# Optimization experiments

Hardware: AMD Instinct MI355X
Metric: run time of the kernel (lower is better)

Reference implementation:

```python
import jax, jax.numpy as jnp
import numpy as np

N = 65536   # base nodes
M = 65536   # union local nodes
E = 1048576 # base edges
EL = 1048576 # local edges
K = 131072  # membership entries
F = 128     # in_channels
H = 128     # hidden_dim
L = 2       # num_layers
OUT = 2
ALPHA = 0.9


def setup_inputs() -> dict:
    key = jax.random.key(0)
    ks = jax.random.split(key, 16)
    s = 1.0 / np.sqrt(H)
    return {
        "x": jax.random.normal(ks[0], (N, F), jnp.float32),
        "edge_index": jax.random.randint(ks[1], (2, E), 0, N, jnp.int64 if jax.config.jax_enable_x64 else jnp.int32),
        "edge_weight": jax.random.uniform(ks[2], (E,), jnp.float32),
        "local_x0": jax.random.normal(ks[3], (M, F), jnp.float32),
        "copy2orig": jax.random.randint(ks[4], (M,), 0, N),
        "local_adj_index": jax.random.randint(ks[5], (2, EL), 0, M),
        "local_adj_value": jax.random.uniform(ks[6], (EL,), jnp.float32),
        "memb_idx": jax.random.randint(ks[7], (K,), 0, M),
        "memb_gid": jax.random.randint(ks[8], (K,), 0, 64),
        "B": 64,
        "Wb_in": jax.random.normal(ks[9], (F, H), jnp.float32) * s,
        "bb_in": jnp.zeros((H,), jnp.float32),
        "Wl_in": jax.random.normal(ks[10], (F, H), jnp.float32) * s,
        "bl_in": jnp.zeros((H,), jnp.float32),
        "W_base": jax.random.normal(ks[11], (L, H, H), jnp.float32) * s,
        "b_base": jnp.zeros((L, H), jnp.float32),
        "W_local": jax.random.normal(ks[12], (L, H, H), jnp.float32) * s,
        "b_local": jnp.zeros((L, H), jnp.float32),
        "Wp": jax.random.normal(ks[13], (H, OUT), jnp.float32) * s,
        "bp": jnp.zeros((OUT,), jnp.float32),
    }


def reference(x, edge_index, edge_weight, local_x0, copy2orig, local_adj_index,
              local_adj_value, memb_idx, memb_gid, B, Wb_in, bb_in, Wl_in, bl_in,
              W_base, b_base, W_local, b_local, Wp, bp):
    n = x.shape[0]
    m = local_x0.shape[0]
    # input projections (dropout is identity in eval mode)
    base_x = jax.nn.relu(x @ Wb_in + bb_in)
    local_x = jax.nn.relu(local_x0 @ Wl_in + bl_in)
    src, dst = edge_index[0], edge_index[1]
    lsrc, ldst = local_adj_index[0], local_adj_index[1]
    for l in range(W_base.shape[0]):
        # base graph propagation: normalized-adjacency spmm then linear+relu
        base_agg = jax.ops.segment_sum(base_x[src] * edge_weight[:, None], dst, num_segments=n)
        base_x = jax.nn.relu(base_agg @ W_base[l] + b_base[l])
        # local union-graph propagation + alpha-mix with base features via copy2orig
        local_agg = jax.ops.segment_sum(local_x[lsrc] * local_adj_value[:, None], ldst, num_segments=m)
        mix = ALPHA * local_agg + (1.0 - ALPHA) * base_x[copy2orig]
        local_x = jax.nn.relu(mix @ W_local[l] + b_local[l])
    # scatter-mean pooling by membership (fused sum + count)
    sub = jax.ops.segment_sum(local_x[memb_idx], memb_gid, num_segments=B)
    cnt = jax.ops.segment_sum(jnp.ones((memb_gid.shape[0], 1), local_x.dtype), memb_gid, num_segments=B)
    sub = sub / jnp.maximum(cnt, 1.0)
    return sub @ Wp + bp
```

## Files before the change

kernel.cpp:

```cpp
#include <hip/hip_runtime.h>

typedef __attribute__((ext_vector_type(8))) short bfrag;
typedef __attribute__((ext_vector_type(4))) float ffrag;

__device__ __forceinline__ ushort f2bf(float f) {
    union { float f; unsigned u; } v{f};
    unsigned r = v.u + 0x7fff + ((v.u >> 16) & 1);
    return (ushort)(r >> 16);
}
__device__ __forceinline__ float bf2f(ushort u) {
    union { unsigned u; float f; } v{(unsigned)u << 16};
    return v.f;
}
__device__ __forceinline__ float bflo(unsigned u) {
    union { unsigned u; float f; } v{u << 16};
    return v.f;
}
__device__ __forceinline__ float bfhi(unsigned u) {
    union { unsigned u; float f; } v{u & 0xffff0000u};
    return v.f;
}


__global__ __launch_bounds__(256) void zero_kernel(int* __restrict__ p, int n) {
    int i = blockIdx.x * 256 + threadIdx.x;
    if (i < n) p[i] = 0;
}


__global__ __launch_bounds__(256) void bhist(const int* __restrict__ dst, int* __restrict__ bcount) {
    __shared__ int h[256];
    const int t = threadIdx.x;
    h[t] = 0;
    __syncthreads();
    const int base = blockIdx.x * 4096;
#pragma unroll
    for (int u = 0; u < 16; ++u)
        atomicAdd(&h[((unsigned)dst[base + u * 256 + t]) >> 8], 1);
    __syncthreads();
    atomicAdd(&bcount[t], h[t]);
}

__global__ __launch_bounds__(256) void bscan(const int* __restrict__ bcount, int* __restrict__ bstart,
                                             int* __restrict__ bcursor) {
    __shared__ int s[256];
    const int t = threadIdx.x;
    int c = bcount[t];
    s[t] = c;
    __syncthreads();
    for (int o = 1; o < 256; o <<= 1) {
        int add = (t >= o) ? s[t - o] : 0;
        __syncthreads();
        s[t] += add;
        __syncthreads();
    }
    int excl = s[t] - c;
    bstart[t] = excl;
    bcursor[t] = excl;
    if (t == 255) bstart[256] = s[t];
}

#define CH 4096

__global__ __launch_bounds__(256) void bucket1(const int* __restrict__ src, const int* __restrict__ dst,
                                               const float* __restrict__ w, int* __restrict__ bcursor,
                                               int2* __restrict__ staged) {
    __shared__ int cnt_s[256], base_l[256], base_g[256], cur[256];
    __shared__ int2 stage[CH];
    __shared__ unsigned char bb[CH];
    const int t = threadIdx.x;
    const int base = blockIdx.x * CH;
    cnt_s[t] = 0;
    __syncthreads();
#pragma unroll
    for (int u = 0; u < CH / 256; ++u) {
        int b = ((unsigned)dst[base + u * 256 + t]) >> 8;
        atomicAdd(&cnt_s[b], 1);
    }
    __syncthreads();
    int v = cnt_s[t];
    base_l[t] = v;
    __syncthreads();
    for (int o = 1; o < 256; o <<= 1) {
        int add = (t >= o) ? base_l[t - o] : 0;
        __syncthreads();
        base_l[t] += add;
        __syncthreads();
    }
    int excl = base_l[t] - v;
    base_l[t] = excl;
    cur[t] = excl;
    base_g[t] = atomicAdd(&bcursor[t], v);
    __syncthreads();
#pragma unroll
    for (int u = 0; u < CH / 256; ++u) {
        int e = base + u * 256 + t;
        int d = dst[e];
        int b = ((unsigned)d) >> 8;
        int p = atomicAdd(&cur[b], 1);
        stage[p] = make_int2((src[e] & 0xffff) | ((d & 255) << 16), __float_as_int(w[e]));
        bb[p] = (unsigned char)b;
    }
    __syncthreads();
    for (int i = t; i < CH; i += 256) {
        int b = bb[i];
        staged[base_g[b] + (i - base_l[b])] = stage[i];
    }
}

__global__ __launch_bounds__(256) void bucket2n(const int* __restrict__ bstart, const int2* __restrict__ staged,
                                                int* __restrict__ start, int2* __restrict__ edges) {
    __shared__ int cnt[256], excl[256], cur[256];
    const int t = threadIdx.x;
    const int b = blockIdx.x;
    cnt[t] = 0;
    __syncthreads();
    const int s0 = bstart[b];
    const int s1 = bstart[b + 1];
    for (int i = s0 + t; i < s1; i += 256) {
        int dl = (staged[i].x >> 16) & 0xff;
        atomicAdd(&cnt[dl], 1);
    }
    __syncthreads();
    int v = cnt[t];
    excl[t] = v;
    __syncthreads();
    for (int o = 1; o < 256; o <<= 1) {
        int add = (t >= o) ? excl[t - o] : 0;
        __syncthreads();
        excl[t] += add;
        __syncthreads();
    }
    int e = excl[t] - v;
    cur[t] = e;
    start[b * 256 + t] = s0 + e;
    if (b == 255 && t == 255) start[256 * 256] = s1;
    __syncthreads();
    for (int i = s0 + t; i < s1; i += 256) {
        int2 se = staged[i];
        int dl = (se.x >> 16) & 0xff;
        int p = s0 + atomicAdd(&cur[dl], 1);
        edges[p] = make_int2(se.x & 0xffff, se.y);
    }
}


__global__ __launch_bounds__(256) void wprep(const float* __restrict__ Wb_in, const float* __restrict__ Wl_in,
                                             const float* __restrict__ W_base, const float* __restrict__ W_local,
                                             ushort* __restrict__ out) {
    int idx = blockIdx.x * 256 + threadIdx.x;
    int mat = idx >> 14;
    int i = idx & 16383;
    int nn = i >> 7, kk = i & 127;
    const float* src;
    switch (mat) {
        case 0: src = Wb_in; break;
        case 1: src = Wl_in; break;
        case 2: src = W_base; break;
        case 3: src = W_base + 16384; break;
        case 4: src = W_local; break;
        default: src = W_local + 16384; break;
    }
    out[(size_t)mat * 16384 + i] = f2bf(src[kk * 128 + nn]);
}


#define ASTRIDE 136

template <bool A_F32, bool MIX>
__global__ __launch_bounds__(256) void gemm_mfma(const void* __restrict__ Ap, const ushort* __restrict__ A2,
                                                 const int* __restrict__ ridx,
                                                 const ushort* __restrict__ Wt, const float* __restrict__ bias,
                                                 ushort* __restrict__ Y) {
    __shared__ ushort As[64 * ASTRIDE];
    __shared__ ushort Bs[128 * ASTRIDE];
    const int tid = threadIdx.x;
    const int r0 = blockIdx.x * 64;

    if (A_F32) {
        const float* A = (const float*)Ap;
#pragma unroll
        for (int p = 0; p < 8; ++p) {
            int c = p * 256 + tid;
            int row = c >> 5, o4 = (c & 31) * 4;
            float4 v = *(const float4*)(A + (size_t)(r0 + row) * 128 + o4);
            ushort4 u;
            u.x = f2bf(v.x); u.y = f2bf(v.y); u.z = f2bf(v.z); u.w = f2bf(v.w);
            *(ushort4*)&As[row * ASTRIDE + o4] = u;
        }
    } else {
        const ushort* A = (const ushort*)Ap;
#pragma unroll
        for (int p = 0; p < 4; ++p) {
            int c = p * 256 + tid;
            int row = c >> 4, o8 = (c & 15) * 8;
            uint4 v = *(const uint4*)(A + (size_t)(r0 + row) * 128 + o8);
            if (MIX) {
                int rr = ridx[r0 + row];
                uint4 v2 = *(const uint4*)(A2 + (size_t)rr * 128 + o8);
                uint4 o;
                float x0, x1;
                x0 = 0.9f * bflo(v.x) + 0.1f * bflo(v2.x);
                x1 = 0.9f * bfhi(v.x) + 0.1f * bfhi(v2.x);
                o.x = (unsigned)f2bf(x0) | ((unsigned)f2bf(x1) << 16);
                x0 = 0.9f * bflo(v.y) + 0.1f * bflo(v2.y);
                x1 = 0.9f * bfhi(v.y) + 0.1f * bfhi(v2.y);
                o.y = (unsigned)f2bf(x0) | ((unsigned)f2bf(x1) << 16);
                x0 = 0.9f * bflo(v.z) + 0.1f * bflo(v2.z);
                x1 = 0.9f * bfhi(v.z) + 0.1f * bfhi(v2.z);
                o.z = (unsigned)f2bf(x0) | ((unsigned)f2bf(x1) << 16);
                x0 = 0.9f * bflo(v.w) + 0.1f * bflo(v2.w);
                x1 = 0.9f * bfhi(v.w) + 0.1f * bfhi(v2.w);
                o.w = (unsigned)f2bf(x0) | ((unsigned)f2bf(x1) << 16);
                v = o;
            }
            *(uint4*)&As[row * ASTRIDE + o8] = v;
        }
    }
#pragma unroll
    for (int p = 0; p < 8; ++p) {
        int c = p * 256 + tid;
        int n = c >> 4, o8 = (c & 15) * 8;
        *(uint4*)&Bs[n * ASTRIDE + o8] = *(const uint4*)(Wt + n * 128 + o8);
    }
    __syncthreads();

    const int lane = tid & 63;
    const int w = tid >> 6;
    const int wm = (w & 1) * 32;
    const int wn = (w >> 1) * 64;
    const int q = lane >> 4;
    const int l16 = lane & 15;

    ffrag acc[2][4];
#pragma unroll
    for (int mt = 0; mt < 2; ++mt)
#pragma unroll
        for (int nt = 0; nt < 4; ++nt) acc[mt][nt] = (ffrag){0.f, 0.f, 0.f, 0.f};

#pragma unroll
    for (int kc = 0; kc < 4; ++kc) {
        bfrag a[2], b[4];
#pragma unroll
        for (int mt = 0; mt < 2; ++mt)
            a[mt] = *(const bfrag*)&As[(wm + mt * 16 + l16) * ASTRIDE + kc * 32 + q * 8];
#pragma unroll
        for (int nt = 0; nt < 4; ++nt)
            b[nt] = *(const bfrag*)&Bs[(wn + nt * 16 + l16) * ASTRIDE + kc * 32 + q * 8];
#pragma unroll
        for (int mt = 0; mt < 2; ++mt)
#pragma unroll
            for (int nt = 0; nt < 4; ++nt)
                acc[mt][nt] = __builtin_amdgcn_mfma_f32_16x16x32_bf16(a[mt], b[nt], acc[mt][nt], 0, 0, 0);
    }

    float bias_v[4];
#pragma unroll
    for (int nt = 0; nt < 4; ++nt) bias_v[nt] = bias[wn + nt * 16 + l16];
#pragma unroll
    for (int mt = 0; mt < 2; ++mt)
#pragma unroll
        for (int nt = 0; nt < 4; ++nt)
#pragma unroll
            for (int r = 0; r < 4; ++r) {
                int row = r0 + wm + mt * 16 + q * 4 + r;
                int col = wn + nt * 16 + l16;
                float v = fmaxf(acc[mt][nt][r] + bias_v[nt], 0.f);
                Y[(size_t)row * 128 + col] = f2bf(v);
            }
}


__global__ __launch_bounds__(256) void spmm_bf16(const int* __restrict__ start, const int2* __restrict__ edges,
                                                 const ushort* __restrict__ X, ushort* __restrict__ Y, int n) {
    int node = (blockIdx.x * 256 + threadIdx.x) >> 5;
    int lane = threadIdx.x & 31;
    if (node >= n) return;
    int s0 = start[node];
    int s1 = start[node + 1];
    const int f = lane * 4;
    float a0 = 0.f, a1 = 0.f, a2 = 0.f, a3 = 0.f;
    int e = s0;
    for (; e + 4 <= s1; e += 4) {
        int2 e0 = edges[e + 0], e1 = edges[e + 1], e2 = edges[e + 2], e3 = edges[e + 3];
        float w0 = __int_as_float(e0.y), w1 = __int_as_float(e1.y);
        float w2 = __int_as_float(e2.y), w3 = __int_as_float(e3.y);
        ushort4 v0 = *(const ushort4*)(X + (size_t)e0.x * 128 + f);
        ushort4 v1 = *(const ushort4*)(X + (size_t)e1.x * 128 + f);
        ushort4 v2 = *(const ushort4*)(X + (size_t)e2.x * 128 + f);
        ushort4 v3 = *(const ushort4*)(X + (size_t)e3.x * 128 + f);
        a0 += w0 * bf2f(v0.x) + w1 * bf2f(v1.x) + w2 * bf2f(v2.x) + w3 * bf2f(v3.x);
        a1 += w0 * bf2f(v0.y) + w1 * bf2f(v1.y) + w2 * bf2f(v2.y) + w3 * bf2f(v3.y);
        a2 += w0 * bf2f(v0.z) + w1 * bf2f(v1.z) + w2 * bf2f(v2.z) + w3 * bf2f(v3.z);
        a3 += w0 * bf2f(v0.w) + w1 * bf2f(v1.w) + w2 * bf2f(v2.w) + w3 * bf2f(v3.w);
    }
    for (; e < s1; ++e) {
        int2 ee = edges[e];
        float w = __int_as_float(ee.y);
        ushort4 v = *(const ushort4*)(X + (size_t)ee.x * 128 + f);
        a0 += w * bf2f(v.x);
        a1 += w * bf2f(v.y);
        a2 += w * bf2f(v.z);
        a3 += w * bf2f(v.w);
    }
    ushort4 o;
    o.x = f2bf(a0);
    o.y = f2bf(a1);
    o.z = f2bf(a2);
    o.w = f2bf(a3);
    *(ushort4*)(Y + (size_t)node * 128 + f) = o;
}


__global__ __launch_bounds__(256) void pool_hist(const int* __restrict__ memb_gid, int* __restrict__ gcount) {
    __shared__ int h[64];
    int t = threadIdx.x;
    if (t < 64) h[t] = 0;
    __syncthreads();
    int base = blockIdx.x * 1024;
#pragma unroll
    for (int u = 0; u < 4; ++u) atomicAdd(&h[memb_gid[base + u * 256 + t]], 1);
    __syncthreads();
    if (t < 64) atomicAdd(&gcount[t], h[t]);
}

__global__ __launch_bounds__(64) void pool_scan(const int* __restrict__ gcount, int* __restrict__ gstart,
                                                int* __restrict__ cursor) {
    __shared__ int s[64];
    int t = threadIdx.x;
    int c = gcount[t];
    s[t] = c;
    __syncthreads();
    int acc = 0;
    for (int j = 0; j < 64; ++j)
        if (j < t) acc += s[j];
    gstart[t] = acc;
    cursor[t] = acc;
    if (t == 63) gstart[64] = acc + c;
}

__global__ __launch_bounds__(256) void pool_scatter(const int* __restrict__ memb_idx,
                                                    const int* __restrict__ memb_gid,
                                                    int* __restrict__ cursor, int* __restrict__ sorted_idx) {
    __shared__ int lhist[64];
    __shared__ int lbase[64];
    __shared__ int loff[1024];
    int t = threadIdx.x;
    if (t < 64) lhist[t] = 0;
    __syncthreads();
    int base = blockIdx.x * 1024;
    int g[4], ix[4];
#pragma unroll
    for (int u = 0; u < 4; ++u) {
        int e = base + u * 256 + t;
        g[u] = memb_gid[e];
        ix[u] = memb_idx[e];
        loff[u * 256 + t] = atomicAdd(&lhist[g[u]], 1);
    }
    __syncthreads();
    if (t < 64) lbase[t] = atomicAdd(&cursor[t], lhist[t]);
    __syncthreads();
#pragma unroll
    for (int u = 0; u < 4; ++u) {
        int pos = lbase[g[u]] + loff[u * 256 + t];
        sorted_idx[pos] = ix[u];
    }
}

__global__ __launch_bounds__(256) void pool_accum(const int* __restrict__ gstart, const int* __restrict__ sorted_idx,
                                                  const ushort* __restrict__ X, float* __restrict__ gsum) {
    const int g = blockIdx.x >> 5;
    const int sgm = blockIdx.x & 31;
    const int gs = gstart[g];
    const int cnt = gstart[g + 1] - gs;
    const int e_begin = gs + ((cnt * sgm) >> 5);
    const int e_end = gs + ((cnt * (sgm + 1)) >> 5);
    const int t = threadIdx.x;
    const int fp = t & 63;
    const int sub = t >> 6;
    float ax = 0.f, ay = 0.f;
#pragma unroll 4
    for (int e = e_begin + sub; e < e_end; e += 4) {
        int idx = sorted_idx[e];
        ushort2 u = *(const ushort2*)(X + (size_t)idx * 128 + fp * 2);
        ax += bf2f(u.x);
        ay += bf2f(u.y);
    }
    __shared__ float sx[256], sy[256];
    sx[t] = ax;
    sy[t] = ay;
    __syncthreads();
    if (t < 64) {
        atomicAdd(&gsum[g * 128 + fp * 2 + 0], sx[t] + sx[t + 64] + sx[t + 128] + sx[t + 192]);
        atomicAdd(&gsum[g * 128 + fp * 2 + 1], sy[t] + sy[t + 64] + sy[t + 128] + sy[t + 192]);
    }
}


__global__ __launch_bounds__(128) void final_kernel(const float* __restrict__ gsum, const int* __restrict__ gcnt,
                                                    const float* __restrict__ Wp, const float* __restrict__ bp,
                                                    float* __restrict__ out) {
    int t = threadIdx.x;
    int g = t >> 1;
    int o = t & 1;
    float inv = 1.f / fmaxf((float)gcnt[g], 1.f);
    float acc = bp[o];
    for (int f = 0; f < 128; ++f) acc += gsum[g * 128 + f] * inv * Wp[f * 2 + o];
    out[g * 2 + o] = acc;
}


extern "C" void kernel_launch(void* const* d_in, const int* in_sizes, int n_in,
                              void* d_out, int out_size, void* d_ws, size_t ws_size,
                              hipStream_t stream) {
    const float* x              = (const float*)d_in[0];
    const int*   edge_index     = (const int*)d_in[1];
    const float* edge_weight    = (const float*)d_in[2];
    const float* local_x0       = (const float*)d_in[3];
    const int*   copy2orig      = (const int*)d_in[4];
    const int*   local_adj_idx  = (const int*)d_in[5];
    const float* local_adj_val  = (const float*)d_in[6];
    const int*   memb_idx       = (const int*)d_in[7];
    const int*   memb_gid       = (const int*)d_in[8];
    const float* Wb_in          = (const float*)d_in[10];
    const float* bb_in          = (const float*)d_in[11];
    const float* Wl_in          = (const float*)d_in[12];
    const float* bl_in          = (const float*)d_in[13];
    const float* W_base         = (const float*)d_in[14];
    const float* b_base         = (const float*)d_in[15];
    const float* W_local        = (const float*)d_in[16];
    const float* b_local        = (const float*)d_in[17];
    const float* Wp             = (const float*)d_in[18];
    const float* bp             = (const float*)d_in[19];
    float* out = (float*)d_out;

    constexpr int N = 65536, M = 65536, E = 1048576, EL = 1048576, K = 131072, H = 128;

    char* wsb = (char*)d_ws;
    size_t off = 0;
    auto alloc = [&](size_t bytes) -> char* {
        char* p = wsb + off;
        off += (bytes + 255) & ~(size_t)255;
        return p;
    };
    int*    bs_start = (int*)alloc((size_t)(N + 1) * 4);
    int2*   bs_edges = (int2*)alloc((size_t)E * 8);
    int2*   bs_stage = (int2*)alloc((size_t)E * 8);
    int*    bs_bcnt  = (int*)alloc(256 * 4);
    int*    bs_bsta  = (int*)alloc(257 * 4);
    int*    bs_bcur  = (int*)alloc(256 * 4);
    int*    ls_start = (int*)alloc((size_t)(M + 1) * 4);
    int2*   ls_edges = (int2*)alloc((size_t)EL * 8);
    int2*   ls_stage = (int2*)alloc((size_t)EL * 8);
    int*    ls_bcnt  = (int*)alloc(256 * 4);
    int*    ls_bsta  = (int*)alloc(257 * 4);
    int*    ls_bcur  = (int*)alloc(256 * 4);
    ushort* bufA     = (ushort*)alloc((size_t)N * H * 2);
    ushort* bufB     = (ushort*)alloc((size_t)M * H * 2);
    ushort* bufC     = (ushort*)alloc((size_t)N * H * 2);
    ushort* bufD     = (ushort*)alloc((size_t)M * H * 2);
    ushort* wt       = (ushort*)alloc((size_t)6 * 16384 * 2);
    int*    p_gcnt   = (int*)alloc(64 * 4);
    int*    p_gstart = (int*)alloc(65 * 4);
    int*    p_cursor = (int*)alloc(64 * 4);
    int*    p_sorted = (int*)alloc((size_t)K * 4);
    float*  pool_sum = (float*)alloc(64 * 128 * 4);

    const int* b_src = edge_index;
    const int* b_dst = edge_index + E;
    const int* l_src = local_adj_idx;
    const int* l_dst = local_adj_idx + EL;

    zero_kernel<<<1, 256, 0, stream>>>(bs_bcnt, 256);
    zero_kernel<<<1, 256, 0, stream>>>(ls_bcnt, 256);
    zero_kernel<<<1, 256, 0, stream>>>(p_gcnt, 64);
    zero_kernel<<<32, 256, 0, stream>>>((int*)pool_sum, 64 * 128);

    wprep<<<384, 256, 0, stream>>>(Wb_in, Wl_in, W_base, W_local, wt);

    bhist<<<E / 4096, 256, 0, stream>>>(b_dst, bs_bcnt);
    bscan<<<1, 256, 0, stream>>>(bs_bcnt, bs_bsta, bs_bcur);
    bucket1<<<E / CH, 256, 0, stream>>>(b_src, b_dst, edge_weight, bs_bcur, bs_stage);
    bucket2n<<<256, 256, 0, stream>>>(bs_bsta, bs_stage, bs_start, bs_edges);

    bhist<<<EL / 4096, 256, 0, stream>>>(l_dst, ls_bcnt);
    bscan<<<1, 256, 0, stream>>>(ls_bcnt, ls_bsta, ls_bcur);
    bucket1<<<EL / CH, 256, 0, stream>>>(l_src, l_dst, local_adj_val, ls_bcur, ls_stage);
    bucket2n<<<256, 256, 0, stream>>>(ls_bsta, ls_stage, ls_start, ls_edges);

    pool_hist<<<K / 1024, 256, 0, stream>>>(memb_gid, p_gcnt);
    pool_scan<<<1, 64, 0, stream>>>(p_gcnt, p_gstart, p_cursor);
    pool_scatter<<<K / 1024, 256, 0, stream>>>(memb_idx, memb_gid, p_cursor, p_sorted);

    gemm_mfma<true, false><<<N / 64, 256, 0, stream>>>(x, nullptr, nullptr, wt, bb_in, bufA);
    gemm_mfma<true, false><<<M / 64, 256, 0, stream>>>(local_x0, nullptr, nullptr, wt + 16384, bl_in, bufB);

    for (int l = 0; l < 2; ++l) {
        spmm_bf16<<<N * 32 / 256, 256, 0, stream>>>(bs_start, bs_edges, bufA, bufC, N);
        spmm_bf16<<<M * 32 / 256, 256, 0, stream>>>(ls_start, ls_edges, bufB, bufD, M);
        gemm_mfma<false, false><<<N / 64, 256, 0, stream>>>(bufC, nullptr, nullptr,
                                                            wt + (size_t)(2 + l) * 16384, b_base + (size_t)l * H, bufA);
        gemm_mfma<false, true><<<M / 64, 256, 0, stream>>>(bufD, bufA, copy2orig,
                                                           wt + (size_t)(4 + l) * 16384, b_local + (size_t)l * H, bufB);
    }

    pool_accum<<<64 * 32, 256, 0, stream>>>(p_gstart, p_sorted, bufB, pool_sum);
    final_kernel<<<1, 128, 0, stream>>>(pool_sum, p_gcnt, Wp, bp, out);
}
```

Baseline: 481.6 us.

## Merge zero kernels, halve bucket chunk size, read GEMM weights from global

Replaces four zeroing launches with a single kernel, cutting launch overhead. Halves the bucketing chunk size (CH) so bucket1 runs with more blocks and less shared memory each. The GEMM no longer stages the weight tile in shared memory and instead reads B fragments straight from global/L2, which raises occupancy but risks uncoalesced, repeated global loads. The bf16 unpack helpers are also replaced with equivalent bf2f calls.

```diff
diff --git a/kernel.cpp b/kernel.cpp
--- a/kernel.cpp
+++ b/kernel.cpp
@@ -12,19 +12,14 @@
     union { unsigned u; float f; } v{(unsigned)u << 16};
     return v.f;
 }
-__device__ __forceinline__ float bflo(unsigned u) {
-    union { unsigned u; float f; } v{u << 16};
-    return v.f;
-}
-__device__ __forceinline__ float bfhi(unsigned u) {
-    union { unsigned u; float f; } v{u & 0xffff0000u};
-    return v.f;
-}
-
-
-__global__ __launch_bounds__(256) void zero_kernel(int* __restrict__ p, int n) {
+
+
+__global__ __launch_bounds__(256) void zero_all(int* __restrict__ a, int* __restrict__ b,
+                                                int* __restrict__ c, int* __restrict__ d) {
     int i = blockIdx.x * 256 + threadIdx.x;
-    if (i < n) p[i] = 0;
+    if (i < 256) { a[i] = 0; b[i] = 0; }
+    if (i < 64) c[i] = 0;
+    if (i < 64 * 128) d[i] = 0;
 }
 
 
@@ -60,7 +55,7 @@
     if (t == 255) bstart[256] = s[t];
 }
 
-#define CH 4096
+#define CH 2048
 
 __global__ __launch_bounds__(256) void bucket1(const int* __restrict__ src, const int* __restrict__ dst,
                                                const float* __restrict__ w, int* __restrict__ bcursor,
@@ -164,8 +159,8 @@
     out[(size_t)mat * 16384 + i] = f2bf(src[kk * 128 + nn]);
 }
 
-
 #define ASTRIDE 136
+
 
 template <bool A_F32, bool MIX>
 __global__ __launch_bounds__(256) void gemm_mfma(const void* __restrict__ Ap, const ushort* __restrict__ A2,
@@ -173,7 +168,6 @@
                                                  const ushort* __restrict__ Wt, const float* __restrict__ bias,
                                                  ushort* __restrict__ Y) {
     __shared__ ushort As[64 * ASTRIDE];
-    __shared__ ushort Bs[128 * ASTRIDE];
     const int tid = threadIdx.x;
     const int r0 = blockIdx.x * 64;
 
@@ -200,28 +194,22 @@
                 uint4 v2 = *(const uint4*)(A2 + (size_t)rr * 128 + o8);
                 uint4 o;
                 float x0, x1;
-                x0 = 0.9f * bflo(v.x) + 0.1f * bflo(v2.x);
-                x1 = 0.9f * bfhi(v.x) + 0.1f * bfhi(v2.x);
+                x0 = 0.9f * bf2f((ushort)(v.x & 0xffff)) + 0.1f * bf2f((ushort)(v2.x & 0xffff));
+                x1 = 0.9f * bf2f((ushort)(v.x >> 16)) + 0.1f * bf2f((ushort)(v2.x >> 16));
                 o.x = (unsigned)f2bf(x0) | ((unsigned)f2bf(x1) << 16);
-                x0 = 0.9f * bflo(v.y) + 0.1f * bflo(v2.y);
-                x1 = 0.9f * bfhi(v.y) + 0.1f * bfhi(v2.y);
+                x0 = 0.9f * bf2f((ushort)(v.y & 0xffff)) + 0.1f * bf2f((ushort)(v2.y & 0xffff));
+                x1 = 0.9f * bf2f((ushort)(v.y >> 16)) + 0.1f * bf2f((ushort)(v2.y >> 16));
                 o.y = (unsigned)f2bf(x0) | ((unsigned)f2bf(x1) << 16);
-                x0 = 0.9f * bflo(v.z) + 0.1f * bflo(v2.z);
-                x1 = 0.9f * bfhi(v.z) + 0.1f * bfhi(v2.z);
+                x0 = 0.9f * bf2f((ushort)(v.z & 0xffff)) + 0.1f * bf2f((ushort)(v2.z & 0xffff));
+                x1 = 0.9f * bf2f((ushort)(v.z >> 16)) + 0.1f * bf2f((ushort)(v2.z >> 16));
                 o.z = (unsigned)f2bf(x0) | ((unsigned)f2bf(x1) << 16);
-                x0 = 0.9f * bflo(v.w) + 0.1f * bflo(v2.w);
-                x1 = 0.9f * bfhi(v.w) + 0.1f * bfhi(v2.w);
+                x0 = 0.9f * bf2f((ushort)(v.w & 0xffff)) + 0.1f * bf2f((ushort)(v2.w & 0xffff));
+                x1 = 0.9f * bf2f((ushort)(v.w >> 16)) + 0.1f * bf2f((ushort)(v2.w >> 16));
                 o.w = (unsigned)f2bf(x0) | ((unsigned)f2bf(x1) << 16);
                 v = o;
             }
             *(uint4*)&As[row * ASTRIDE + o8] = v;
         }
-    }
-#pragma unroll
-    for (int p = 0; p < 8; ++p) {
-        int c = p * 256 + tid;
-        int n = c >> 4, o8 = (c & 15) * 8;
-        *(uint4*)&Bs[n * ASTRIDE + o8] = *(const uint4*)(Wt + n * 128 + o8);
     }
     __syncthreads();
 
@@ -246,7 +234,7 @@
             a[mt] = *(const bfrag*)&As[(wm + mt * 16 + l16) * ASTRIDE + kc * 32 + q * 8];
 #pragma unroll
         for (int nt = 0; nt < 4; ++nt)
-            b[nt] = *(const bfrag*)&Bs[(wn + nt * 16 + l16) * ASTRIDE + kc * 32 + q * 8];
+            b[nt] = *(const bfrag*)(Wt + (wn + nt * 16 + l16) * 128 + kc * 32 + q * 8);
 #pragma unroll
         for (int mt = 0; mt < 2; ++mt)
 #pragma unroll
@@ -471,10 +459,7 @@
     const int* l_src = local_adj_idx;
     const int* l_dst = local_adj_idx + EL;
 
-    zero_kernel<<<1, 256, 0, stream>>>(bs_bcnt, 256);
-    zero_kernel<<<1, 256, 0, stream>>>(ls_bcnt, 256);
-    zero_kernel<<<1, 256, 0, stream>>>(p_gcnt, 64);
-    zero_kernel<<<32, 256, 0, stream>>>((int*)pool_sum, 64 * 128);
+    zero_all<<<32, 256, 0, stream>>>(bs_bcnt, ls_bcnt, p_gcnt, (int*)pool_sum);
 
     wprep<<<384, 256, 0, stream>>>(Wb_in, Wl_in, W_base, W_local, wt);
 
```

Result: slower. 510.6 us (+6.0%).
